# Performance work log

Measured on AMD Instinct MI355X. Metric: run time of the kernel, lower is better.

Reference implementation:

```python
import jax, jax.numpy as jnp
import numpy as np

N = 100000
E = 1600000
F_IN = 64
DIM = 64
OUT = 10
NUM_GRAPHS = 1000
BN_EPS = 1e-5


def gcn_conv(x, W, b, src, dst, n):
    # PyG GCNConv: add self-loops, symmetric normalization, scatter-add.
    h = x @ W                                   # [N, dim]
    ones = jnp.ones(src.shape[0], dtype=x.dtype)
    deg = jax.ops.segment_sum(ones, dst, num_segments=n) + 1.0  # +1 self-loop
    dinv = jax.lax.rsqrt(deg)                   # deg^{-1/2}
    msg = h[src] * (dinv[src] * dinv[dst])[:, None]  # [E, dim]
    out = jax.ops.segment_sum(msg, dst, num_segments=n)
    out = out + h * (dinv * dinv)[:, None]      # self-loop term
    return out + b


def batchnorm_eval(x, gamma, beta, mean, var):
    return (x - mean) * jax.lax.rsqrt(var + BN_EPS) * gamma + beta


def setup_inputs() -> dict:
    key = jax.random.key(0)
    ks = jax.random.split(key, 16)
    x = jax.random.normal(ks[0], (N, F_IN), dtype=jnp.float32)
    edge_index = jax.random.randint(ks[1], (2, E), 0, N)
    batch = jnp.sort(jax.random.randint(ks[2], (N,), 0, NUM_GRAPHS))

    def lin(k, fan_in, fan_out):
        s = 1.0 / np.sqrt(fan_in)
        kw, kb = jax.random.split(k)
        W = jax.random.uniform(kw, (fan_in, fan_out), minval=-s, maxval=s, dtype=jnp.float32)
        b = jax.random.uniform(kb, (fan_out,), minval=-s, maxval=s, dtype=jnp.float32)
        return W, b

    W1, b1 = lin(ks[3], F_IN, DIM)
    W2, b2 = lin(ks[4], DIM, DIM)
    W3, b3 = lin(ks[5], DIM, DIM)
    W4, b4 = lin(ks[6], DIM, DIM)
    lin1_W, lin1_b = lin(ks[7], 4 * DIM, DIM)
    lin2_W, lin2_b = lin(ks[8], DIM, OUT)

    bn_gamma = jnp.ones((4, DIM), dtype=jnp.float32)
    bn_beta = jnp.zeros((4, DIM), dtype=jnp.float32)
    bn_mean = jnp.zeros((4, DIM), dtype=jnp.float32)
    bn_var = jnp.ones((4, DIM), dtype=jnp.float32)

    return {
        'x': x, 'edge_index': edge_index, 'batch': batch, 'num_graphs': NUM_GRAPHS,
        'W1': W1, 'b1': b1, 'W2': W2, 'b2': b2, 'W3': W3, 'b3': b3, 'W4': W4, 'b4': b4,
        'bn_gamma': bn_gamma, 'bn_beta': bn_beta, 'bn_mean': bn_mean, 'bn_var': bn_var,
        'lin1_W': lin1_W, 'lin1_b': lin1_b, 'lin2_W': lin2_W, 'lin2_b': lin2_b,
    }


def reference(x, edge_index, batch, num_graphs, W1, b1, W2, b2, W3, b3, W4, b4,
              bn_gamma, bn_beta, bn_mean, bn_var, lin1_W, lin1_b, lin2_W, lin2_b):
    src, dst = edge_index[0], edge_index[1]
    n = x.shape[0]
    Ws = [(W1, b1), (W2, b2), (W3, b3), (W4, b4)]
    xs = []
    h = x
    for i, (W, b) in enumerate(Ws):
        h = gcn_conv(h, W, b, src, dst, n)
        h = batchnorm_eval(h, bn_gamma[i], bn_beta[i], bn_mean[i], bn_var[i])
        h = jax.nn.relu(h)
        xs.append(h)
    h = jnp.concatenate(xs, axis=-1)                         # JK 'cat' -> [N, 4*dim]
    pooled = jax.ops.segment_sum(h, batch, num_segments=num_graphs)  # [G, 4*dim]
    # dropout is identity in eval mode
    out = jax.nn.relu(pooled @ lin1_W + lin1_b)
    out = out @ lin2_W + lin2_b
    return out
```

## Files before the change

### kernel.cpp

```cpp
#include <hip/hip_runtime.h>
#include <hip/hip_bf16.h>

#define N_NODES   100000
#define N_EDGES   1600000
#define DIM       64
#define OUT_DIM   10
#define N_GRAPHS  1000
#define BN_EPS    1e-5f
#define NBUCKET   391
#define TILE_E    6400
#define NT        250

typedef __hip_bfloat16 bf16;
__device__ __forceinline__ float b2f(bf16 v) { return __bfloat162float(v); }

typedef __attribute__((ext_vector_type(8))) short short8;
typedef __attribute__((ext_vector_type(4))) float floatx4;

__device__ __forceinline__ short f2bs(float f) {
    union { bf16 h; short s; } u;
    u.h = __float2bfloat16(f);
    return u.s;
}


__global__ void __launch_bounds__(256) k_bucket_count(const int* __restrict__ dst,
                                                      int* __restrict__ tileCnt, int e) {
    __shared__ int hcnt[NBUCKET];
    int t = blockIdx.x, tid = threadIdx.x;
    for (int b = tid; b < NBUCKET; b += 256) hcnt[b] = 0;
    __syncthreads();
    int ibase = t * TILE_E;
    for (int j = 0; j < TILE_E; j += 256) {
        int i = ibase + j + tid;
        if (i < e) atomicAdd(&hcnt[dst[i] >> 8], 1);
    }
    __syncthreads();
    for (int b = tid; b < NBUCKET; b += 256) tileCnt[b * NT + t] = hcnt[b];
}


__global__ void __launch_bounds__(256) k_tile_scan(int* __restrict__ tileCnt,
                                                   int* __restrict__ bucketTot) {
    __shared__ int tmp[256];
    int b = blockIdx.x, tid = threadIdx.x;
    int v = (tid < NT) ? tileCnt[b * NT + tid] : 0;
    tmp[tid] = v;
    __syncthreads();
    for (int off = 1; off < 256; off <<= 1) {
        int t = (tid >= off) ? tmp[tid - off] : 0;
        __syncthreads();
        tmp[tid] += t;
        __syncthreads();
    }
    if (tid < NT) tileCnt[b * NT + tid] = tmp[tid] - v;
    if (tid == 255) bucketTot[b] = tmp[255];
}


__global__ void k_scan_sums(int* __restrict__ bsums, int nb) {
    __shared__ int tmp[512];
    int tid = threadIdx.x;
    int v = (tid < nb) ? bsums[tid] : 0;
    tmp[tid] = v;
    __syncthreads();
    for (int off = 1; off < 512; off <<= 1) {
        int t = (tid >= off) ? tmp[tid - off] : 0;
        __syncthreads();
        tmp[tid] += t;
        __syncthreads();
    }
    if (tid < nb) bsums[tid] = tmp[tid] - v;
}


__global__ void __launch_bounds__(256) k_bucket_write(
    const int* __restrict__ src, const int* __restrict__ dst,
    const int* __restrict__ bbase, const int* __restrict__ tilePrefix,
    unsigned int* __restrict__ packed, int e) {
    __shared__ int hbase[NBUCKET];
    __shared__ int hcur[NBUCKET];
    int t = blockIdx.x, tid = threadIdx.x;
    for (int b = tid; b < NBUCKET; b += 256) {
        hbase[b] = bbase[b] + tilePrefix[b * NT + t];
        hcur[b] = 0;
    }
    __syncthreads();
    int ibase = t * TILE_E;
    for (int j = 0; j < TILE_E; j += 256) {
        int i = ibase + j + tid;
        if (i < e) {
            int d  = dst[i];
            int bb = d >> 8;
            int pos = hbase[bb] + atomicAdd(&hcur[bb], 1);
            packed[pos] = ((unsigned int)src[i] << 8) | (unsigned int)(d & 255);
        }
    }
}


__global__ void __launch_bounds__(256) k_local_sort(
    const unsigned int* __restrict__ packed, const int* __restrict__ bbase,
    int* __restrict__ ssrc, int* __restrict__ offs, int* __restrict__ hist,
    float* __restrict__ dinv, int n, int e) {
    __shared__ int tmp[256];
    __shared__ int noffs[256];
    __shared__ int ncur[256];
    int b = blockIdx.x, tid = threadIdx.x;
    int base   = b << 8;
    int estart = bbase[b];
    int eend   = (b + 1 < NBUCKET) ? bbase[b + 1] : e;

    ncur[tid] = 0;
    __syncthreads();
    for (int i = estart + tid; i < eend; i += 256)
        atomicAdd(&ncur[packed[i] & 255u], 1);
    __syncthreads();
    int v = ncur[tid];
    tmp[tid] = v;
    __syncthreads();
    for (int off = 1; off < 256; off <<= 1) {
        int t = (tid >= off) ? tmp[tid - off] : 0;
        __syncthreads();
        tmp[tid] += t;
        __syncthreads();
    }
    int mystart = estart + tmp[tid] - v;
    noffs[tid] = mystart;
    ncur[tid]  = 0;
    int node = base + tid;
    if (node < n) {
        offs[node] = mystart;
        hist[node] = v;
        dinv[node] = rsqrtf((float)(v + 1));
    }
    __syncthreads();
    for (int i = estart + tid; i < eend; i += 256) {
        unsigned int p = packed[i];
        int d = p & 255u;
        int pos = noffs[d] + atomicAdd(&ncur[d], 1);
        ssrc[pos] = (int)(p >> 8);
    }
}


__global__ void __launch_bounds__(256) k_matmul_mfma(
    const float* __restrict__ hf, const bf16* __restrict__ hb, int use_f32,
    const float* __restrict__ W, const float* __restrict__ dinv,
    bf16* __restrict__ Hs, int ntiles, int nwaves)
{
    int wid  = (blockIdx.x * blockDim.x + threadIdx.x) >> 6;
    int lane = threadIdx.x & 63;
    if (wid >= ntiles) return;
    int quad = lane >> 4, m16 = lane & 15;

    short8 Bfrag[4][2];
#pragma unroll
    for (int t = 0; t < 4; t++)
#pragma unroll
        for (int h = 0; h < 2; h++) {
            short8 b;
#pragma unroll
            for (int j = 0; j < 8; j++)
                b[j] = f2bs(W[(h * 32 + quad * 8 + j) * 64 + t * 16 + m16]);
            Bfrag[t][h] = b;
        }

    for (int tile = wid; tile < ntiles; tile += nwaves) {
        int row0 = tile * 16;
        short8 A0, A1;
        if (use_f32) {
            const float* base = hf + (size_t)(row0 + m16) * 64 + quad * 8;
#pragma unroll
            for (int j = 0; j < 8; j++) {
                A0[j] = f2bs(base[j]);
                A1[j] = f2bs(base[32 + j]);
            }
        } else {
            const short* base = (const short*)hb + (size_t)(row0 + m16) * 64 + quad * 8;
            A0 = *(const short8*)(base);
            A1 = *(const short8*)(base + 32);
        }

        floatx4 acc[4];
#pragma unroll
        for (int t = 0; t < 4; t++) {
            floatx4 c = {0.f, 0.f, 0.f, 0.f};
            c = __builtin_amdgcn_mfma_f32_16x16x32_bf16(A0, Bfrag[t][0], c, 0, 0, 0);
            c = __builtin_amdgcn_mfma_f32_16x16x32_bf16(A1, Bfrag[t][1], c, 0, 0, 0);
            acc[t] = c;
        }

#pragma unroll
        for (int r = 0; r < 4; r++) {
            int row = row0 + quad * 4 + r;
            float dn = dinv[row];
#pragma unroll
            for (int t = 0; t < 4; t++)
                Hs[(size_t)row * 64 + t * 16 + m16] = __float2bfloat16(dn * acc[t][r]);
        }
    }
}


__global__ void __launch_bounds__(256) k_gather(
    const bf16* __restrict__ Hs, const int* __restrict__ ssrc,
    const int* __restrict__ offs, const int* __restrict__ hist,
    const float* __restrict__ dinv, const float* __restrict__ bias,
    const float* __restrict__ gamma, const float* __restrict__ beta,
    const float* __restrict__ mean, const float* __restrict__ var,
    const int* __restrict__ batch, bf16* __restrict__ hout,
    float* __restrict__ pooled, int layer, int n, int nwaves)
{
    int wid  = (blockIdx.x * blockDim.x + threadIdx.x) >> 6;
    int lane = threadIdx.x & 63;

    float P = gamma[lane] * rsqrtf(var[lane] + BN_EPS);
    float Q = (bias[lane] - mean[lane]) * P + beta[lane];

    for (int node = wid; node < n; node += nwaves) {
        int start = __builtin_amdgcn_readfirstlane(offs[node]);
        int cnt   = __builtin_amdgcn_readfirstlane(hist[node]);

        float acc = b2f(Hs[node * 64 + lane]);
        int i = 0;
        for (; i + 15 < cnt; i += 16) {
            int s0  = ssrc[start + i];
            int s1  = ssrc[start + i + 1];
            int s2  = ssrc[start + i + 2];
            int s3  = ssrc[start + i + 3];
            int s4  = ssrc[start + i + 4];
            int s5  = ssrc[start + i + 5];
            int s6  = ssrc[start + i + 6];
            int s7  = ssrc[start + i + 7];
            int s8  = ssrc[start + i + 8];
            int s9  = ssrc[start + i + 9];
            int s10 = ssrc[start + i + 10];
            int s11 = ssrc[start + i + 11];
            int s12 = ssrc[start + i + 12];
            int s13 = ssrc[start + i + 13];
            int s14 = ssrc[start + i + 14];
            int s15 = ssrc[start + i + 15];
            float v0  = b2f(Hs[s0  * 64 + lane]);
            float v1  = b2f(Hs[s1  * 64 + lane]);
            float v2  = b2f(Hs[s2  * 64 + lane]);
            float v3  = b2f(Hs[s3  * 64 + lane]);
            float v4  = b2f(Hs[s4  * 64 + lane]);
            float v5  = b2f(Hs[s5  * 64 + lane]);
            float v6  = b2f(Hs[s6  * 64 + lane]);
            float v7  = b2f(Hs[s7  * 64 + lane]);
            float v8  = b2f(Hs[s8  * 64 + lane]);
            float v9  = b2f(Hs[s9  * 64 + lane]);
            float v10 = b2f(Hs[s10 * 64 + lane]);
            float v11 = b2f(Hs[s11 * 64 + lane]);
            float v12 = b2f(Hs[s12 * 64 + lane]);
            float v13 = b2f(Hs[s13 * 64 + lane]);
            float v14 = b2f(Hs[s14 * 64 + lane]);
            float v15 = b2f(Hs[s15 * 64 + lane]);
            acc += (((v0 + v1) + (v2 + v3)) + ((v4 + v5) + (v6 + v7))) +
                   (((v8 + v9) + (v10 + v11)) + ((v12 + v13) + (v14 + v15)));
        }
        for (; i + 7 < cnt; i += 8) {
            int s0 = ssrc[start + i];
            int s1 = ssrc[start + i + 1];
            int s2 = ssrc[start + i + 2];
            int s3 = ssrc[start + i + 3];
            int s4 = ssrc[start + i + 4];
            int s5 = ssrc[start + i + 5];
            int s6 = ssrc[start + i + 6];
            int s7 = ssrc[start + i + 7];
            float v0 = b2f(Hs[s0 * 64 + lane]);
            float v1 = b2f(Hs[s1 * 64 + lane]);
            float v2 = b2f(Hs[s2 * 64 + lane]);
            float v3 = b2f(Hs[s3 * 64 + lane]);
            float v4 = b2f(Hs[s4 * 64 + lane]);
            float v5 = b2f(Hs[s5 * 64 + lane]);
            float v6 = b2f(Hs[s6 * 64 + lane]);
            float v7 = b2f(Hs[s7 * 64 + lane]);
            acc += ((v0 + v1) + (v2 + v3)) + ((v4 + v5) + (v6 + v7));
        }
        for (; i + 3 < cnt; i += 4) {
            int s0 = ssrc[start + i];
            int s1 = ssrc[start + i + 1];
            int s2 = ssrc[start + i + 2];
            int s3 = ssrc[start + i + 3];
            float v0 = b2f(Hs[s0 * 64 + lane]);
            float v1 = b2f(Hs[s1 * 64 + lane]);
            float v2 = b2f(Hs[s2 * 64 + lane]);
            float v3 = b2f(Hs[s3 * 64 + lane]);
            acc += (v0 + v1) + (v2 + v3);
        }
        for (; i < cnt; i++)
            acc += b2f(Hs[ssrc[start + i] * 64 + lane]);

        float val = fmaxf(dinv[node] * acc * P + Q, 0.f);

        atomicAdd(&pooled[batch[node] * 256 + layer * 64 + lane], val);

        if (hout) hout[node * 64 + lane] = __float2bfloat16(val);
    }
}


__global__ void k_mlp(const float* __restrict__ pooled, const float* __restrict__ W1,
                      const float* __restrict__ b1, const float* __restrict__ W2,
                      const float* __restrict__ b2, float* __restrict__ out) {
    __shared__ float p[256];
    __shared__ float t[64];
    int g = blockIdx.x;
    int tid = threadIdx.x;
    for (int i = tid; i < 256; i += 64) p[i] = pooled[g * 256 + i];
    __syncthreads();
    float acc = b1[tid];
    for (int k = 0; k < 256; k++)
        acc = fmaf(p[k], W1[k * 64 + tid], acc);
    t[tid] = fmaxf(acc, 0.f);
    __syncthreads();
    if (tid < OUT_DIM) {
        float o = b2[tid];
#pragma unroll
        for (int d = 0; d < 64; d++)
            o = fmaf(t[d], W2[d * OUT_DIM + tid], o);
        out[g * OUT_DIM + tid] = o;
    }
}


extern "C" void kernel_launch(void* const* d_in, const int* in_sizes, int n_in,
                              void* d_out, int out_size, void* d_ws, size_t ws_size,
                              hipStream_t stream) {
    const float* x          = (const float*)d_in[0];
    const int*   edge_index = (const int*)d_in[1];
    const int*   batch      = (const int*)d_in[2];
    const float* Wl[4] = { (const float*)d_in[4], (const float*)d_in[6],
                           (const float*)d_in[8], (const float*)d_in[10] };
    const float* bl[4] = { (const float*)d_in[5], (const float*)d_in[7],
                           (const float*)d_in[9], (const float*)d_in[11] };
    const float* bn_gamma = (const float*)d_in[12];
    const float* bn_beta  = (const float*)d_in[13];
    const float* bn_mean  = (const float*)d_in[14];
    const float* bn_var   = (const float*)d_in[15];
    const float* lin1_W = (const float*)d_in[16];
    const float* lin1_b = (const float*)d_in[17];
    const float* lin2_W = (const float*)d_in[18];
    const float* lin2_b = (const float*)d_in[19];

    const int* src = edge_index;
    const int* dst = edge_index + N_EDGES;

    char* p = (char*)d_ws;
    auto alloc = [&](size_t bytes) {
        char* r = p;
        p += (bytes + 255) & ~(size_t)255;
        return (void*)r;
    };
    bf16*  Hs     = (bf16*) alloc((size_t)N_NODES * 64 * 2);
    bf16*  hbuf   = (bf16*) alloc((size_t)N_NODES * 64 * 2);
    int*   hist   = (int*)  alloc((size_t)N_NODES * 4);
    int*   offs   = (int*)  alloc((size_t)N_NODES * 4);
    float* dinv   = (float*)alloc((size_t)N_NODES * 4);
    int*   ssrc   = (int*)  alloc((size_t)N_EDGES * 4);
    unsigned int* packed = (unsigned int*)alloc((size_t)N_EDGES * 4);
    int*   tileCnt   = (int*)alloc((size_t)NBUCKET * NT * 4);
    int*   bucketTot = (int*)alloc((size_t)NBUCKET * 4);
    float* pooled = (float*)alloc((size_t)N_GRAPHS * 256 * 4);

    hipMemsetAsync(pooled, 0, (size_t)N_GRAPHS * 256 * 4, stream);

    k_bucket_count<<<NT, 256, 0, stream>>>(dst, tileCnt, N_EDGES);
    k_tile_scan<<<NBUCKET, 256, 0, stream>>>(tileCnt, bucketTot);
    k_scan_sums<<<1, 512, 0, stream>>>(bucketTot, NBUCKET);
    k_bucket_write<<<NT, 256, 0, stream>>>(src, dst, bucketTot, tileCnt, packed, N_EDGES);
    k_local_sort<<<NBUCKET, 256, 0, stream>>>(packed, bucketTot, ssrc, offs, hist,
                                              dinv, N_NODES, N_EDGES);

    const int mmTiles  = N_NODES / 16;
    const int mmBlocks = (mmTiles + 3) / 4;
    const int mmWaves  = mmBlocks * 4;

    k_matmul_mfma<<<mmBlocks, 256, 0, stream>>>(x, (const bf16*)nullptr, 1,
                                                Wl[0], dinv, Hs, mmTiles, mmWaves);

    const int gatherBlocks = 4096;
    const int nwaves = gatherBlocks * 4;
    for (int layer = 0; layer < 4; layer++) {
        bf16* hout = (layer < 3) ? hbuf : (bf16*)nullptr;
        k_gather<<<gatherBlocks, 256, 0, stream>>>(
            Hs, ssrc, offs, hist, dinv, bl[layer],
            bn_gamma + layer * 64, bn_beta + layer * 64,
            bn_mean + layer * 64, bn_var + layer * 64,
            batch, hout, pooled, layer, N_NODES, nwaves);
        if (layer < 3)
            k_matmul_mfma<<<mmBlocks, 256, 0, stream>>>((const float*)nullptr, hbuf, 0,
                                                        Wl[layer + 1], dinv, Hs,
                                                        mmTiles, mmWaves);
    }

    k_mlp<<<N_GRAPHS, 64, 0, stream>>>(pooled, lin1_W, lin1_b, lin2_W, lin2_b,
                                       (float*)d_out);
}
```

Baseline: 430.8 us.

## Fuse GCN gather with next layer's MFMA matmul via shared-memory tile

For layers 0-2, the neighbour gather/BN/ReLU is fused with the following layer's 64x64 bf16 MFMA matmul. Each block gathers 16 nodes into an LDS tile, then applies W and writes the next Hs directly, alternating between two ping-pong buffers. This removes the intermediate hbuf write/read and three separate matmul launches. In exchange, each gather block now has two __syncthreads per tile and fewer, more persistent blocks (2048), which may reduce latency hiding for the random gathers. The first matmul grid is also cut to 512 persistent blocks.

```diff
diff --git a/kernel.cpp b/kernel.cpp
--- a/kernel.cpp
+++ b/kernel.cpp
@@ -145,9 +145,8 @@
 
 
 __global__ void __launch_bounds__(256) k_matmul_mfma(
-    const float* __restrict__ hf, const bf16* __restrict__ hb, int use_f32,
-    const float* __restrict__ W, const float* __restrict__ dinv,
-    bf16* __restrict__ Hs, int ntiles, int nwaves)
+    const float* __restrict__ hf, const float* __restrict__ W,
+    const float* __restrict__ dinv, bf16* __restrict__ Hs, int ntiles, int nwaves)
 {
     int wid  = (blockIdx.x * blockDim.x + threadIdx.x) >> 6;
     int lane = threadIdx.x & 63;
@@ -169,17 +168,11 @@
     for (int tile = wid; tile < ntiles; tile += nwaves) {
         int row0 = tile * 16;
         short8 A0, A1;
-        if (use_f32) {
-            const float* base = hf + (size_t)(row0 + m16) * 64 + quad * 8;
-#pragma unroll
-            for (int j = 0; j < 8; j++) {
-                A0[j] = f2bs(base[j]);
-                A1[j] = f2bs(base[32 + j]);
-            }
-        } else {
-            const short* base = (const short*)hb + (size_t)(row0 + m16) * 64 + quad * 8;
-            A0 = *(const short8*)(base);
-            A1 = *(const short8*)(base + 32);
+        const float* base = hf + (size_t)(row0 + m16) * 64 + quad * 8;
+#pragma unroll
+        for (int j = 0; j < 8; j++) {
+            A0[j] = f2bs(base[j]);
+            A1[j] = f2bs(base[32 + j]);
         }
 
         floatx4 acc[4];
@@ -199,6 +192,112 @@
             for (int t = 0; t < 4; t++)
                 Hs[(size_t)row * 64 + t * 16 + m16] = __float2bfloat16(dn * acc[t][r]);
         }
+    }
+}
+
+
+__global__ void __launch_bounds__(256) k_gather_mm(
+    const bf16* __restrict__ HsIn, const int* __restrict__ ssrc,
+    const int* __restrict__ offs, const int* __restrict__ hist,
+    const float* __restrict__ dinv, const float* __restrict__ bias,
+    const float* __restrict__ gamma, const float* __restrict__ beta,
+    const float* __restrict__ mean, const float* __restrict__ var,
+    const int* __restrict__ batch, const float* __restrict__ W,
+    bf16* __restrict__ HsOut, float* __restrict__ pooled, int layer, int ntiles)
+{
+    __shared__ short tile[16][72];
+    int wv   = threadIdx.x >> 6;
+    int lane = threadIdx.x & 63;
+    int quad = lane >> 4, m16 = lane & 15;
+
+    float P = gamma[lane] * rsqrtf(var[lane] + BN_EPS);
+    float Q = (bias[lane] - mean[lane]) * P + beta[lane];
+
+    short8 B0, B1;
+#pragma unroll
+    for (int j = 0; j < 8; j++) {
+        B0[j] = f2bs(W[(quad * 8 + j) * 64 + wv * 16 + m16]);
+        B1[j] = f2bs(W[(32 + quad * 8 + j) * 64 + wv * 16 + m16]);
+    }
+
+    for (int t = blockIdx.x; t < ntiles; t += gridDim.x) {
+        int row0 = t * 16;
+#pragma unroll
+        for (int j2 = 0; j2 < 4; j2++) {
+            int node = row0 + wv * 4 + j2;
+            int start = __builtin_amdgcn_readfirstlane(offs[node]);
+            int cnt   = __builtin_amdgcn_readfirstlane(hist[node]);
+
+            float acc = b2f(HsIn[node * 64 + lane]);
+            int i = 0;
+            for (; i + 15 < cnt; i += 16) {
+                int s0  = ssrc[start + i];
+                int s1  = ssrc[start + i + 1];
+                int s2  = ssrc[start + i + 2];
+                int s3  = ssrc[start + i + 3];
+                int s4  = ssrc[start + i + 4];
+                int s5  = ssrc[start + i + 5];
+                int s6  = ssrc[start + i + 6];
+                int s7  = ssrc[start + i + 7];
+                int s8  = ssrc[start + i + 8];
+                int s9  = ssrc[start + i + 9];
+                int s10 = ssrc[start + i + 10];
+                int s11 = ssrc[start + i + 11];
+                int s12 = ssrc[start + i + 12];
+                int s13 = ssrc[start + i + 13];
+                int s14 = ssrc[start + i + 14];
+                int s15 = ssrc[start + i + 15];
+                float v0  = b2f(HsIn[s0  * 64 + lane]);
+                float v1  = b2f(HsIn[s1  * 64 + lane]);
+                float v2  = b2f(HsIn[s2  * 64 + lane]);
+                float v3  = b2f(HsIn[s3  * 64 + lane]);
+                float v4  = b2f(HsIn[s4  * 64 + lane]);
+                float v5  = b2f(HsIn[s5  * 64 + lane]);
+                float v6  = b2f(HsIn[s6  * 64 + lane]);
+                float v7  = b2f(HsIn[s7  * 64 + lane]);
+                float v8  = b2f(HsIn[s8  * 64 + lane]);
+                float v9  = b2f(HsIn[s9  * 64 + lane]);
+                float v10 = b2f(HsIn[s10 * 64 + lane]);
+                float v11 = b2f(HsIn[s11 * 64 + lane]);
+                float v12 = b2f(HsIn[s12 * 64 + lane]);
+                float v13 = b2f(HsIn[s13 * 64 + lane]);
+                float v14 = b2f(HsIn[s14 * 64 + lane]);
+                float v15 = b2f(HsIn[s15 * 64 + lane]);
+                acc += (((v0 + v1) + (v2 + v3)) + ((v4 + v5) + (v6 + v7))) +
+                       (((v8 + v9) + (v10 + v11)) + ((v12 + v13) + (v14 + v15)));
+            }
+            for (; i + 3 < cnt; i += 4) {
+                int s0 = ssrc[start + i];
+                int s1 = ssrc[start + i + 1];
+                int s2 = ssrc[start + i + 2];
+                int s3 = ssrc[start + i + 3];
+                float v0 = b2f(HsIn[s0 * 64 + lane]);
+                float v1 = b2f(HsIn[s1 * 64 + lane]);
+                float v2 = b2f(HsIn[s2 * 64 + lane]);
+                float v3 = b2f(HsIn[s3 * 64 + lane]);
+                acc += (v0 + v1) + (v2 + v3);
+            }
+            for (; i < cnt; i++)
+                acc += b2f(HsIn[ssrc[start + i] * 64 + lane]);
+
+            float val = fmaxf(dinv[node] * acc * P + Q, 0.f);
+            atomicAdd(&pooled[batch[node] * 256 + layer * 64 + lane], val);
+            tile[wv * 4 + j2][lane] = f2bs(val);
+        }
+        __syncthreads();
+
+        short8 A0 = *(const short8*)&tile[m16][quad * 8];
+        short8 A1 = *(const short8*)&tile[m16][32 + quad * 8];
+        floatx4 c = {0.f, 0.f, 0.f, 0.f};
+        c = __builtin_amdgcn_mfma_f32_16x16x32_bf16(A0, B0, c, 0, 0, 0);
+        c = __builtin_amdgcn_mfma_f32_16x16x32_bf16(A1, B1, c, 0, 0, 0);
+#pragma unroll
+        for (int r = 0; r < 4; r++) {
+            int row = row0 + quad * 4 + r;
+            HsOut[(size_t)row * 64 + wv * 16 + m16] =
+                __float2bfloat16(dinv[row] * c[r]);
+        }
+        __syncthreads();
     }
 }
 
@@ -209,8 +308,8 @@
     const float* __restrict__ dinv, const float* __restrict__ bias,
     const float* __restrict__ gamma, const float* __restrict__ beta,
     const float* __restrict__ mean, const float* __restrict__ var,
-    const int* __restrict__ batch, bf16* __restrict__ hout,
-    float* __restrict__ pooled, int layer, int n, int nwaves)
+    const int* __restrict__ batch, float* __restrict__ pooled,
+    int layer, int n, int nwaves)
 {
     int wid  = (blockIdx.x * blockDim.x + threadIdx.x) >> 6;
     int lane = threadIdx.x & 63;
@@ -294,10 +393,7 @@
             acc += b2f(Hs[ssrc[start + i] * 64 + lane]);
 
         float val = fmaxf(dinv[node] * acc * P + Q, 0.f);
-
         atomicAdd(&pooled[batch[node] * 256 + layer * 64 + lane], val);
-
-        if (hout) hout[node * 64 + lane] = __float2bfloat16(val);
     }
 }
 
@@ -354,8 +450,8 @@
         p += (bytes + 255) & ~(size_t)255;
         return (void*)r;
     };
-    bf16*  Hs     = (bf16*) alloc((size_t)N_NODES * 64 * 2);
-    bf16*  hbuf   = (bf16*) alloc((size_t)N_NODES * 64 * 2);
+    bf16*  HsA    = (bf16*) alloc((size_t)N_NODES * 64 * 2);
+    bf16*  HsB    = (bf16*) alloc((size_t)N_NODES * 64 * 2);
     int*   hist   = (int*)  alloc((size_t)N_NODES * 4);
     int*   offs   = (int*)  alloc((size_t)N_NODES * 4);
     float* dinv   = (float*)alloc((size_t)N_NODES * 4);
@@ -375,26 +471,25 @@
                                               dinv, N_NODES, N_EDGES);
 
     const int mmTiles  = N_NODES / 16;
-    const int mmBlocks = (mmTiles + 3) / 4;
+    const int mmBlocks = 512;
     const int mmWaves  = mmBlocks * 4;
 
-    k_matmul_mfma<<<mmBlocks, 256, 0, stream>>>(x, (const bf16*)nullptr, 1,
-                                                Wl[0], dinv, Hs, mmTiles, mmWaves);
-
-    const int gatherBlocks = 4096;
-    const int nwaves = gatherBlocks * 4;
-    for (int layer = 0; layer < 4; layer++) {
-        bf16* hout = (layer < 3) ? hbuf : (bf16*)nullptr;
-        k_gather<<<gatherBlocks, 256, 0, stream>>>(
-            Hs, ssrc, offs, hist, dinv, bl[layer],
+    k_matmul_mfma<<<mmBlocks, 256, 0, stream>>>(x, Wl[0], dinv, HsA, mmTiles, mmWaves);
+
+    bf16* hsIn[3]  = { HsA, HsB, HsA };
+    bf16* hsOut[3] = { HsB, HsA, HsB };
+    for (int layer = 0; layer < 3; layer++) {
+        k_gather_mm<<<2048, 256, 0, stream>>>(
+            hsIn[layer], ssrc, offs, hist, dinv, bl[layer],
             bn_gamma + layer * 64, bn_beta + layer * 64,
             bn_mean + layer * 64, bn_var + layer * 64,
-            batch, hout, pooled, layer, N_NODES, nwaves);
-        if (layer < 3)
-            k_matmul_mfma<<<mmBlocks, 256, 0, stream>>>((const float*)nullptr, hbuf, 0,
-                                                        Wl[layer + 1], dinv, Hs,
-                                                        mmTiles, mmWaves);
-    }
+            batch, Wl[layer + 1], hsOut[layer], pooled, layer, mmTiles);
+    }
+    k_gather<<<4096, 256, 0, stream>>>(
+        HsB, ssrc, offs, hist, dinv, bl[3],
+        bn_gamma + 3 * 64, bn_beta + 3 * 64,
+        bn_mean + 3 * 64, bn_var + 3 * 64,
+        batch, pooled, 3, N_NODES, 4096 * 4);
 
     k_mlp<<<N_GRAPHS, 64, 0, stream>>>(pooled, lin1_W, lin1_b, lin2_W, lin2_b,
                                        (float*)d_out);
```

Result: slower. 441.0 us (+2.4%).
